# Kernel tuning notes

Measured on AMD Instinct MI355X. Metric: run time of the kernel, lower is better.

The kernel has to match this reference:

```python
import jax, jax.numpy as jnp
import numpy as np

B, N, C, NB, K, CAT = 8, 32768, 32, 2, 22, 40


def setup_inputs() -> dict:
    key = jax.random.key(0)
    ks = jax.random.split(key, 16)
    w = lambda k, s: jax.random.normal(k, s, jnp.float32) * 0.05
    return {
        "features": jax.random.normal(ks[0], (B, 1, N, K), jnp.float32),
        "clusters": jax.random.randint(ks[1], (NB, B, N), 0, C),
        "w_in": w(ks[2], (256, K)), "b_in": jnp.zeros((256,), jnp.float32),
        "w1": w(ks[3], (NB, 64, 256)), "b1": jnp.zeros((NB, 64), jnp.float32),
        "w2": w(ks[4], (NB, 128, 64)), "b2": jnp.zeros((NB, 128), jnp.float32),
        "w3": w(ks[5], (NB, 128, 128)), "b3": jnp.zeros((NB, 128), jnp.float32),
        "wc1": w(ks[6], (NB, 128, 128)), "bc1": jnp.zeros((NB, 128), jnp.float32),
        "wc2": w(ks[7], (NB, 256, 128)), "bc2": jnp.zeros((NB, 256), jnp.float32),
        "wc3": w(ks[8], (NB, 32, 256)), "bc3": jnp.zeros((NB, 32), jnp.float32),
        "w_out1": w(ks[9], (128, 256)), "b_out1": jnp.zeros((128,), jnp.float32),
        "w_out2": w(ks[10], (128, 128)), "b_out2": jnp.zeros((128,), jnp.float32),
        "dw1": w(ks[11], (128, 256)), "db1": jnp.zeros((256,), jnp.float32),
        "dw2": w(ks[12], (256, 256)), "db2": jnp.zeros((256,), jnp.float32),
        "dw3": w(ks[13], (256, CAT)), "db3": jnp.zeros((CAT,), jnp.float32),
    }


def conv(x, w, b):  # 1x1 conv over [B, Cin, N] -> [B, Cout, N] with ReLU
    return jax.nn.relu(jnp.einsum('oc,bcn->bon', w, x) + b[None, :, None])


def seg_max(x, idx):  # x [B, d, N], idx [B, N] -> [B, d, C] (matches masked -100 max-pool)
    f = jax.vmap(lambda xi, ii: jax.ops.segment_max(xi.T, ii, num_segments=C))(x, idx)
    return jnp.maximum(f.transpose(0, 2, 1), -100.0)


def pooling_block(f, idx, wc1, bc1, wc2, bc2, wc3, bc3):
    corr = conv(conv(conv(f, wc1, bc1), wc2, bc2), wc3, bc3)  # [B, 32, N]
    cf = seg_max(f, idx)      # [B, d, C]
    cc = seg_max(corr, idx)   # [B, 32, C]
    cm = cc.transpose(0, 2, 1)  # [B, C, 32]
    cm = cm / jnp.maximum(jnp.linalg.norm(cm, axis=-1, keepdims=True), 1e-12)
    corr_matrix = cm @ cm.transpose(0, 2, 1)  # [B, C, C]
    cf = cf @ corr_matrix  # [B, d, C]
    # scatter-back: each point gathers its cluster's pooled feature
    return jnp.take_along_axis(cf, idx[:, None, :], axis=2)  # [B, d, N]


def reference(features, clusters, w_in, b_in, w1, b1, w2, b2, w3, b3,
              wc1, bc1, wc2, bc2, wc3, bc3, w_out1, b_out1, w_out2, b_out2,
              dw1, db1, dw2, db2, dw3, db3):
    x = features[:, 0]  # [B, N, K]
    f = jax.nn.relu(jnp.einsum('ok,bnk->bon', w_in, x) + b_in[None, :, None])  # [B,256,N]
    for i in range(NB):
        f = conv(f, w1[i], b1[i])   # 256 -> 64
        f = conv(f, w2[i], b2[i])   # 64 -> 128
        pool = pooling_block(f, clusters[i], wc1[i], bc1[i], wc2[i], bc2[i], wc3[i], bc3[i])
        f = conv(f, w3[i], b3[i])   # 128 -> 128
        f = jnp.concatenate([f, pool], axis=1)  # -> 256
    o = conv(conv(f, w_out1, b_out1), w_out2, b_out2)  # [B,128,N]
    net = jnp.max(o, axis=2)  # global max-pool over N -> [B,128]
    lrelu = lambda v: jnp.where(v >= 0, v, 0.2 * v)
    net = lrelu(net @ dw1 + db1)
    net = lrelu(net @ dw2 + db2)
    return net @ dw3 + db3  # [B, CAT]
```

## Files before the change

kernel.cpp:

```cpp
#include <hip/hip_runtime.h>
#include <stdint.h>

#define B_   8
#define N_   32768
#define C_   32
#define K_   22
#define CAT_ 40

typedef unsigned short u16;
typedef unsigned int   u32;

typedef __attribute__((ext_vector_type(8))) short bf16x8;
typedef __attribute__((ext_vector_type(4))) float f32x4;

#define MFMA(a, b, c) __builtin_amdgcn_mfma_f32_16x16x32_bf16(a, b, c, 0, 0, 0)

__device__ __forceinline__ float b2f(u16 v) { return __uint_as_float(((u32)v) << 16); }
__device__ __forceinline__ u16 f2b(float f) {
    u32 x = __float_as_uint(f);
    return (u16)((x + 0x7fffu + ((x >> 16) & 1u)) >> 16);
}
__device__ __forceinline__ u32 pk2(float a, float b) {
    return (u32)f2b(a) | ((u32)f2b(b) << 16);
}

#define PK_WIN 0
#define PK_W1  8192
#define PK_W2  40960
#define PK_W3  57344
#define PK_WC1 90112
#define PK_WC2 122880
#define PK_WC3 188416
#define PK_WO1 204800
#define PK_WO2 237568

#define OBIN 0
#define OB1  256
#define OB2  384
#define OB3  640
#define OBC1 896
#define OBC2 1152
#define OBC3 1664
#define OBO1 1728
#define OBO2 1856
#define ODB1 1984
#define ODB2 2240
#define ODB3 2496

#define ODW1 0
#define ODW2 32768
#define ODW3 98304

#define OFS_WPK   0u
#define OFS_BIAS  524288u
#define OFS_DWC   540672u
#define OFS_MODE  786432u
#define OFS_FEATC 1048576u
#define OFS_GACC0 12582912u
#define OFS_GACC1 12746752u
#define OFS_GNET  12910592u
#define GACC_ZERO_BYTES 331776u
#define OFS_CF2B0 12914688u
#define OFS_CF2B1 12980224u
#define OFS_F0    16777216u
#define OFS_F1    83886080u

#define SEGSTR 161
#define SEGTOT (32 * SEGSTR)
#define CFSTR 136

__global__ void kSniff(const u16* __restrict__ featAny, int* __restrict__ mode) {
    __shared__ int cnt;
    if (threadIdx.x == 0) cnt = 0;
    __syncthreads();
    int weird = 0;
    for (int j = 0; j < 4; ++j) {
        u16 v = featAny[threadIdx.x * 4 + j];
        float f = b2f(v);
        if (v == 0 || !(fabsf(f) < 1e10f)) weird++;
    }
    if (weird) atomicAdd(&cnt, weird);
    __syncthreads();
    if (threadIdx.x == 0) *mode = (cnt > 64) ? 1 : 0;
}

__device__ __forceinline__ float fetchF(const void* src, size_t i, int mode) {
    return mode ? ((const float*)src)[i] : b2f(((const u16*)src)[i]);
}

__device__ void packA(const void* __restrict__ src, u16* __restrict__ dst,
                      int COUT, int CIN, int mode, int tid, int np) {
    int KB = (CIN + 31) / 32;
    int tiles = COUT / 16;
    int tot = tiles * KB * 64 * 8;
    for (int i = tid; i < tot; i += np) {
        int j = i & 7;
        int L = (i >> 3) & 63;
        int rest = i >> 9;
        int kb = rest % KB, tile = rest / KB;
        int co = tile * 16 + (L & 15);
        int ci = kb * 32 + (L >> 4) * 8 + j;
        float v = (ci < CIN) ? fetchF(src, (size_t)co * CIN + ci, mode) : 0.f;
        dst[i] = f2b(v);
    }
}

__device__ void cvtF(const void* __restrict__ src, float* __restrict__ dst,
                     int n, int mode, int tid, int np) {
    for (int i = tid; i < n; i += np) dst[i] = fetchF(src, i, mode);
}

__device__ void cvtB(const void* __restrict__ src, u16* __restrict__ dst,
                     int n, int mode, int tid, int np) {
    for (int i = tid; i < n; i += np)
        dst[i] = mode ? f2b(((const float*)src)[i]) : ((const u16*)src)[i];
}

__global__ void kPrep(const void* feat, const void* w_in, const void* b_in,
                      const void* w1, const void* b1, const void* w2, const void* b2,
                      const void* w3, const void* b3,
                      const void* wc1, const void* bc1, const void* wc2, const void* bc2,
                      const void* wc3, const void* bc3,
                      const void* wo1, const void* bo1, const void* wo2, const void* bo2,
                      const void* dw1, const void* db1, const void* dw2, const void* db2,
                      const void* dw3, const void* db3,
                      u16* WPK, float* BIAS, u16* DWC, u16* FEATC,
                      const int* __restrict__ modep) {
    const int mode = *modep;
    int tid = blockIdx.x * blockDim.x + threadIdx.x;
    int np  = gridDim.x * blockDim.x;
    cvtB(feat, FEATC, B_ * N_ * K_, mode, tid, np);
    packA(w_in, WPK + PK_WIN, 256, 22, mode, tid, np);
    packA(w1,                                 WPK + PK_W1,          64, 256, mode, tid, np);
    packA((const u16*)w1 + (mode?32768:16384), WPK + PK_W1 + 16384,  64, 256, mode, tid, np);
    packA(w2,                                 WPK + PK_W2,          128, 64, mode, tid, np);
    packA((const u16*)w2 + (mode?16384:8192),  WPK + PK_W2 + 8192,   128, 64, mode, tid, np);
    packA(w3,                                 WPK + PK_W3,          128, 128, mode, tid, np);
    packA((const u16*)w3 + (mode?32768:16384), WPK + PK_W3 + 16384,  128, 128, mode, tid, np);
    packA(wc1,                                WPK + PK_WC1,         128, 128, mode, tid, np);
    packA((const u16*)wc1 + (mode?32768:16384),WPK + PK_WC1 + 16384, 128, 128, mode, tid, np);
    packA(wc2,                                WPK + PK_WC2,         256, 128, mode, tid, np);
    packA((const u16*)wc2 + (mode?65536:32768),WPK + PK_WC2 + 32768, 256, 128, mode, tid, np);
    packA(wc3,                                WPK + PK_WC3,         32, 256, mode, tid, np);
    packA((const u16*)wc3 + (mode?16384:8192), WPK + PK_WC3 + 8192,  32, 256, mode, tid, np);
    packA(wo1, WPK + PK_WO1, 128, 256, mode, tid, np);
    packA(wo2, WPK + PK_WO2, 128, 128, mode, tid, np);
    cvtF(b_in, BIAS + OBIN, 256, mode, tid, np);
    cvtF(b1,   BIAS + OB1,  128, mode, tid, np);
    cvtF(b2,   BIAS + OB2,  256, mode, tid, np);
    cvtF(b3,   BIAS + OB3,  256, mode, tid, np);
    cvtF(bc1,  BIAS + OBC1, 256, mode, tid, np);
    cvtF(bc2,  BIAS + OBC2, 512, mode, tid, np);
    cvtF(bc3,  BIAS + OBC3, 64,  mode, tid, np);
    cvtF(bo1,  BIAS + OBO1, 128, mode, tid, np);
    cvtF(bo2,  BIAS + OBO2, 128, mode, tid, np);
    cvtF(db1,  BIAS + ODB1, 256, mode, tid, np);
    cvtF(db2,  BIAS + ODB2, 256, mode, tid, np);
    cvtF(db3,  BIAS + ODB3, 40,  mode, tid, np);
    cvtB(dw1, DWC + ODW1, 128 * 256, mode, tid, np);
    cvtB(dw2, DWC + ODW2, 256 * 256, mode, tid, np);
    cvtB(dw3, DWC + ODW3, 256 * 40,  mode, tid, np);
}

__device__ __forceinline__ void storeRow(u16* __restrict__ buf, int p, int col,
                                         float r0, float r1, float r2, float r3) {
    *(uint2*)(buf + p * 136 + col) = make_uint2(pk2(r0, r1), pk2(r2, r3));
}

template<int NF>
__device__ __forceinline__ void loadWF(const u16* __restrict__ wA, int lane, bf16x8 (&wf)[NF]) {
#pragma unroll
    for (int i = 0; i < NF; ++i)
        wf[i] = *(const bf16x8*)(wA + ((size_t)(i * 64 + lane)) * 8);
}

template<int KB, int INS>
__device__ __forceinline__ void convP128w(const bf16x8 (&wf)[KB], const float* __restrict__ bias,
                                          const u16* __restrict__ sIn, u16* __restrict__ sOut) {
    const int t = threadIdx.x, lane = t & 63, w = t >> 6, lp = lane & 15, q = lane >> 4;
    f32x4 acc[8] = {};
#pragma unroll
    for (int kb = 0; kb < KB; ++kb) {
        bf16x8 bb[8];
#pragma unroll
        for (int pt = 0; pt < 8; ++pt)
            bb[pt] = *(const bf16x8*)(sIn + (pt * 16 + lp) * INS + kb * 32 + q * 8);
#pragma unroll
        for (int pt = 0; pt < 8; ++pt) acc[pt] = MFMA(wf[kb], bb[pt], acc[pt]);
    }
    const int co = w * 16 + q * 4;
    f32x4 bv = *(const f32x4*)(bias + co);
#pragma unroll
    for (int pt = 0; pt < 8; ++pt) {
        f32x4 v = acc[pt];
        storeRow(sOut, pt * 16 + lp, co,
                 fmaxf(v[0] + bv[0], 0.f), fmaxf(v[1] + bv[1], 0.f),
                 fmaxf(v[2] + bv[2], 0.f), fmaxf(v[3] + bv[3], 0.f));
    }
}

__device__ __forceinline__ void convW2_128w(const bf16x8 (&wf)[2], const float* __restrict__ bias,
                                            const u16* __restrict__ sIn, u16* __restrict__ sOut,
                                            const int* __restrict__ sCluSeg, int* __restrict__ sSeg) {
    const int t = threadIdx.x, lane = t & 63, w = t >> 6, lp = lane & 15, q = lane >> 4;
    f32x4 acc[8] = {};
#pragma unroll
    for (int kb = 0; kb < 2; ++kb) {
        bf16x8 bb[8];
#pragma unroll
        for (int pt = 0; pt < 8; ++pt)
            bb[pt] = *(const bf16x8*)(sIn + (pt * 16 + lp) * 136 + kb * 32 + q * 8);
#pragma unroll
        for (int pt = 0; pt < 8; ++pt) acc[pt] = MFMA(wf[kb], bb[pt], acc[pt]);
    }
    const int co = w * 16 + q * 4;
    f32x4 bv = *(const f32x4*)(bias + co);
#pragma unroll
    for (int pt = 0; pt < 8; ++pt) {
        f32x4 v = acc[pt];
        const int p = pt * 16 + lp;
        float r0 = fmaxf(v[0] + bv[0], 0.f), r1 = fmaxf(v[1] + bv[1], 0.f);
        float r2 = fmaxf(v[2] + bv[2], 0.f), r3 = fmaxf(v[3] + bv[3], 0.f);
        *(uint2*)(sOut + p * 136 + co) = make_uint2(pk2(r0, r1), pk2(r2, r3));
        const int sb = sCluSeg[p] * SEGSTR + co;
        atomicMax(&sSeg[sb + 0], __float_as_int(r0));
        atomicMax(&sSeg[sb + 1], __float_as_int(r1));
        atomicMax(&sSeg[sb + 2], __float_as_int(r2));
        atomicMax(&sSeg[sb + 3], __float_as_int(r3));
    }
}

__device__ __forceinline__ void convCat128w(const bf16x8 (&wf)[8], const float* __restrict__ bias,
                                            const u16* __restrict__ sLo, const u16* __restrict__ sHi,
                                            u16* __restrict__ sOut) {
    const int t = threadIdx.x, lane = t & 63, w = t >> 6, lp = lane & 15, q = lane >> 4;
    const int ct = w & 3, pp = (w >> 2) * 4;
    f32x4 acc[4] = {};
#pragma unroll
    for (int kb = 0; kb < 8; ++kb) {
        const u16* sIn = (kb < 4) ? sLo : sHi;
        const int col = (kb & 3) * 32 + q * 8;
        bf16x8 bb[4];
#pragma unroll
        for (int i = 0; i < 4; ++i)
            bb[i] = *(const bf16x8*)(sIn + ((pp + i) * 16 + lp) * 136 + col);
#pragma unroll
        for (int i = 0; i < 4; ++i) acc[i] = MFMA(wf[kb], bb[i], acc[i]);
    }
    const int co = ct * 16 + q * 4;
    f32x4 bv = *(const f32x4*)(bias + co);
#pragma unroll
    for (int i = 0; i < 4; ++i) {
        f32x4 v = acc[i];
        storeRow(sOut, (pp + i) * 16 + lp, co,
                 fmaxf(v[0] + bv[0], 0.f), fmaxf(v[1] + bv[1], 0.f),
                 fmaxf(v[2] + bv[2], 0.f), fmaxf(v[3] + bv[3], 0.f));
    }
}

__device__ __forceinline__ void convCatG128s(const bf16x8 (&wf)[8], const float* __restrict__ bias,
                                             const u16* __restrict__ sIn, const u16* __restrict__ sCf,
                                             const int* __restrict__ sClu, u16* __restrict__ sOut) {
    const int t = threadIdx.x, lane = t & 63, w = t >> 6, lp = lane & 15, q = lane >> 4;
    const int ct = w & 3, pp = (w >> 2) * 4;
    f32x4 acc[4] = {};
#pragma unroll
    for (int kb = 0; kb < 8; ++kb) {
        bf16x8 bb[4];
#pragma unroll
        for (int i = 0; i < 4; ++i) {
            const int p = (pp + i) * 16 + lp;
            if (kb < 4) bb[i] = *(const bf16x8*)(sIn + p * 136 + kb * 32 + q * 8);
            else        bb[i] = *(const bf16x8*)(sCf + sClu[p] * CFSTR + (kb - 4) * 32 + q * 8);
        }
#pragma unroll
        for (int i = 0; i < 4; ++i) acc[i] = MFMA(wf[kb], bb[i], acc[i]);
    }
    const int co = ct * 16 + q * 4;
    f32x4 bv = *(const f32x4*)(bias + co);
#pragma unroll
    for (int i = 0; i < 4; ++i) {
        f32x4 v = acc[i];
        storeRow(sOut, (pp + i) * 16 + lp, co,
                 fmaxf(v[0] + bv[0], 0.f), fmaxf(v[1] + bv[1], 0.f),
                 fmaxf(v[2] + bv[2], 0.f), fmaxf(v[3] + bv[3], 0.f));
    }
}

__device__ __forceinline__ void convG128w(const bf16x8 (&wf)[4], const float* __restrict__ bias,
                                          const u16* __restrict__ gB, u16* __restrict__ sOut) {
    const int t = threadIdx.x, lane = t & 63, w = t >> 6, lp = lane & 15, q = lane >> 4;
    f32x4 acc[8] = {};
#pragma unroll
    for (int kb = 0; kb < 4; ++kb) {
        bf16x8 bb[8];
#pragma unroll
        for (int pt = 0; pt < 8; ++pt)
            bb[pt] = *(const bf16x8*)(gB + pt * 2048 + kb * 512 + lane * 8);
#pragma unroll
        for (int pt = 0; pt < 8; ++pt) acc[pt] = MFMA(wf[kb], bb[pt], acc[pt]);
    }
    const int co = w * 16 + q * 4;
    f32x4 bv = *(const f32x4*)(bias + co);
#pragma unroll
    for (int pt = 0; pt < 8; ++pt) {
        f32x4 v = acc[pt];
        storeRow(sOut, pt * 16 + lp, co,
                 fmaxf(v[0] + bv[0], 0.f), fmaxf(v[1] + bv[1], 0.f),
                 fmaxf(v[2] + bv[2], 0.f), fmaxf(v[3] + bv[3], 0.f));
    }
}

__device__ __forceinline__ void wc3seg128w(const bf16x8 (&wf)[8], const float* __restrict__ bias,
                                           const u16* __restrict__ sLo, const u16* __restrict__ sHi,
                                           const int* __restrict__ sClu, int* __restrict__ sSeg) {
    const int t = threadIdx.x, lane = t & 63, w = t >> 6, lp = lane & 15, q = lane >> 4;
    const int ct = w & 1, pp = (w >> 1) * 2;
    f32x4 acc[2] = {};
#pragma unroll
    for (int kb = 0; kb < 8; ++kb) {
        const u16* sIn = (kb < 4) ? sLo : sHi;
        const int col = (kb & 3) * 32 + q * 8;
        bf16x8 b0 = *(const bf16x8*)(sIn + ((pp + 0) * 16 + lp) * 136 + col);
        bf16x8 b1 = *(const bf16x8*)(sIn + ((pp + 1) * 16 + lp) * 136 + col);
        acc[0] = MFMA(wf[kb], b0, acc[0]);
        acc[1] = MFMA(wf[kb], b1, acc[1]);
    }
    const int col = ct * 16 + q * 4;
    f32x4 bv = *(const f32x4*)(bias + col);
#pragma unroll
    for (int i = 0; i < 2; ++i) {
        const int p = (pp + i) * 16 + lp;
        const int cl = sClu[p];
        f32x4 v = acc[i];
        atomicMax(&sSeg[cl * SEGSTR + 128 + col + 0], __float_as_int(fmaxf(v[0] + bv[0], 0.f)));
        atomicMax(&sSeg[cl * SEGSTR + 128 + col + 1], __float_as_int(fmaxf(v[1] + bv[1], 0.f)));
        atomicMax(&sSeg[cl * SEGSTR + 128 + col + 2], __float_as_int(fmaxf(v[2] + bv[2], 0.f)));
        atomicMax(&sSeg[cl * SEGSTR + 128 + col + 3], __float_as_int(fmaxf(v[3] + bv[3], 0.f)));
    }
}

__device__ __forceinline__ void convCatG128os(const bf16x8 (&wf)[8], const float* __restrict__ bias,
                                              const u16* __restrict__ sIn, const u16* __restrict__ sCf,
                                              const int* __restrict__ sClu, u16* __restrict__ sOut) {
    const int t = threadIdx.x, lane = t & 63, w = t >> 6, lp = lane & 15, q = lane >> 4;
    f32x4 acc[8] = {};
#pragma unroll
    for (int kb = 0; kb < 8; ++kb) {
        bf16x8 bb[8];
#pragma unroll
        for (int pt = 0; pt < 8; ++pt) {
            const int p = pt * 16 + lp;
            if (kb < 4) bb[pt] = *(const bf16x8*)(sIn + p * 136 + kb * 32 + q * 8);
            else        bb[pt] = *(const bf16x8*)(sCf + sClu[p] * CFSTR + (kb - 4) * 32 + q * 8);
        }
#pragma unroll
        for (int pt = 0; pt < 8; ++pt) acc[pt] = MFMA(wf[kb], bb[pt], acc[pt]);
    }
    const int co = w * 16 + q * 4;
    f32x4 bv = *(const f32x4*)(bias + co);
#pragma unroll
    for (int pt = 0; pt < 8; ++pt) {
        f32x4 v = acc[pt];
        storeRow(sOut, pt * 16 + lp, co,
                 fmaxf(v[0] + bv[0], 0.f), fmaxf(v[1] + bv[1], 0.f),
                 fmaxf(v[2] + bv[2], 0.f), fmaxf(v[3] + bv[3], 0.f));
    }
}

__device__ __forceinline__ void convNet128w(const bf16x8 (&wf)[4], const float* __restrict__ bias,
                                            const u16* __restrict__ sIn, int* __restrict__ sNet) {
    const int t = threadIdx.x, lane = t & 63, w = t >> 6, lp = lane & 15, q = lane >> 4;
    f32x4 acc[8] = {};
#pragma unroll
    for (int kb = 0; kb < 4; ++kb) {
        bf16x8 bb[8];
#pragma unroll
        for (int pt = 0; pt < 8; ++pt)
            bb[pt] = *(const bf16x8*)(sIn + (pt * 16 + lp) * 136 + kb * 32 + q * 8);
#pragma unroll
        for (int pt = 0; pt < 8; ++pt) acc[pt] = MFMA(wf[kb], bb[pt], acc[pt]);
    }
    const int co = w * 16 + q * 4;
    f32x4 bv = *(const f32x4*)(bias + co);
    f32x4 m = acc[0];
#pragma unroll
    for (int pt = 1; pt < 8; ++pt) {
        m[0] = fmaxf(m[0], acc[pt][0]); m[1] = fmaxf(m[1], acc[pt][1]);
        m[2] = fmaxf(m[2], acc[pt][2]); m[3] = fmaxf(m[3], acc[pt][3]);
    }
    atomicMax(&sNet[co + 0], __float_as_int(fmaxf(m[0] + bv[0], 0.f)));
    atomicMax(&sNet[co + 1], __float_as_int(fmaxf(m[1] + bv[1], 0.f)));
    atomicMax(&sNet[co + 2], __float_as_int(fmaxf(m[2] + bv[2], 0.f)));
    atomicMax(&sNet[co + 3], __float_as_int(fmaxf(m[3] + bv[3], 0.f)));
}

__global__ __launch_bounds__(512, 2)
void kA0a(const u16* __restrict__ featc, const int* __restrict__ clu0,
          const u16* __restrict__ WPK, const float* __restrict__ BIAS,
          u16* __restrict__ gF, int* __restrict__ gSeg) {
    __shared__ __attribute__((aligned(16))) u16 sA[128 * 136];
    __shared__ __attribute__((aligned(16))) u16 sB[128 * 136];
    __shared__ __attribute__((aligned(16))) u16 sC[128 * 136];
    __shared__ __attribute__((aligned(16))) u16 sFeat[128 * 40];
    __shared__ int sSeg[SEGTOT];
    __shared__ int sClu[128];
    const int t = threadIdx.x, lane = t & 63, w = t >> 6, lp = lane & 15, q = lane >> 4;
    const int b = blockIdx.y;
    const size_t bN = (size_t)b * N_;
    bf16x8 wf1a[1], wf1b[1], wf2[8], wf3[2];
    loadWF(WPK + PK_WIN + w * 512, lane, wf1a);
    loadWF(WPK + PK_WIN + 4096 + w * 512, lane, wf1b);
    loadWF(WPK + PK_W1 + (w & 3) * 4096, lane, wf2);
    loadWF(WPK + PK_W2 + w * 1024, lane, wf3);
    for (int i = t; i < SEGTOT; i += 512) sSeg[i] = 0;
    {
        const int n0 = blockIdx.x * 1024;
        for (int i = t; i < 5120; i += 512) {
            int p = i / 40, k = i - p * 40;
            sFeat[i] = (k < 22) ? featc[(bN + n0 + p) * 22 + k] : (u16)0;
        }
    }
    __syncthreads();
    for (int s = 0; s < 8; ++s) {
        const int n0 = (blockIdx.x * 8 + s) * 128;
        const size_t ntB = (size_t)b * 2048 + (size_t)(blockIdx.x * 8 + s) * 8;
        if (t < 128) sClu[t] = clu0[bN + n0 + t];
        convP128w<1, 40>(wf1a, BIAS + OBIN,       sFeat, sA);
        convP128w<1, 40>(wf1b, BIAS + OBIN + 128, sFeat, sB);
        __syncthreads();
        convCat128w(wf2, BIAS + OB1, sA, sB, sC);
        __syncthreads();
        convW2_128w(wf3, BIAS + OB2, sC, sA, sClu, sSeg);
        __syncthreads();
        {
#pragma unroll
            for (int r = 0; r < 4; ++r) {
                bf16x8 v = *(const bf16x8*)(sA + (w * 16 + lp) * 136 + r * 32 + q * 8);
                *(bf16x8*)(gF + ((ntB + w) * 4 + r) * 512 + lane * 8) = v;
            }
        }
        if (s < 7) {
            const int n1 = n0 + 128;
            for (int i = t; i < 5120; i += 512) {
                int p = i / 40, k = i - p * 40;
                sFeat[i] = (k < 22) ? featc[(bN + n1 + p) * 22 + k] : (u16)0;
            }
        }
        __syncthreads();
    }
    for (int i = t; i < 4096; i += 512) {
        int cl = i >> 7, ch = i & 127;
        atomicMax(&gSeg[b * 5120 + cl * 160 + ch], sSeg[cl * SEGSTR + ch]);
    }
}

template<int PKOFF, int BOFF>
__device__ __forceinline__ void kAbBody(const u16* __restrict__ gFp, const int* __restrict__ clu,
                                        const u16* __restrict__ WPK, const float* __restrict__ BIAS,
                                        int* __restrict__ gSeg) {
    __shared__ __attribute__((aligned(16))) u16 sA[128 * 136];
    __shared__ __attribute__((aligned(16))) u16 sB[128 * 136];
    __shared__ __attribute__((aligned(16))) u16 sC[128 * 136];
    __shared__ int sSeg[SEGTOT];
    __shared__ int sClu[128];
    const int t = threadIdx.x, lane = t & 63, w = t >> 6;
    const int b = blockIdx.y;
    const size_t bN = (size_t)b * N_;
    bf16x8 wf4[4], wf5a[4], wf5b[4], wf6[8];
    loadWF(WPK + PK_WC1 + PKOFF * 16384 + w * 2048, lane, wf4);
    loadWF(WPK + PK_WC2 + PKOFF * 32768 + w * 2048, lane, wf5a);
    loadWF(WPK + PK_WC2 + PKOFF * 32768 + 16384 + w * 2048, lane, wf5b);
    loadWF(WPK + PK_WC3 + PKOFF * 8192 + (w & 1) * 4096, lane, wf6);
    for (int i = t; i < SEGTOT; i += 512) sSeg[i] = 0;
    __syncthreads();
    for (int s = 0; s < 8; ++s) {
        const int n0 = (blockIdx.x * 8 + s) * 128;
        const size_t ntB = (size_t)b * 2048 + (size_t)(blockIdx.x * 8 + s) * 8;
        if (t < 128) sClu[t] = clu[bN + n0 + t];
        const u16* gB = gFp + ntB * 2048;
        convG128w(wf4, BIAS + OBC1 + BOFF * 128, gB, sA);
        __syncthreads();
        convP128w<4, 136>(wf5a, BIAS + OBC2 + BOFF * 256,       sA, sB);
        convP128w<4, 136>(wf5b, BIAS + OBC2 + BOFF * 256 + 128, sA, sC);
        __syncthreads();
        wc3seg128w(wf6, BIAS + OBC3 + BOFF * 32, sB, sC, sClu, sSeg);
        __syncthreads();
    }
    for (int i = t; i < 1024; i += 512) {
        int cl = i >> 5, ch = i & 31;
        atomicMax(&gSeg[b * 5120 + cl * 160 + 128 + ch], sSeg[cl * SEGSTR + 128 + ch]);
    }
}

__global__ __launch_bounds__(512, 2)
void kA0b(const u16* __restrict__ gFp, const int* __restrict__ clu0,
          const u16* __restrict__ WPK, const float* __restrict__ BIAS,
          int* __restrict__ gSeg) {
    kAbBody<0, 0>(gFp, clu0, WPK, BIAS, gSeg);
}

__global__ __launch_bounds__(512, 2)
void kA1b(const u16* __restrict__ gFp, const int* __restrict__ clu1,
          const u16* __restrict__ WPK, const float* __restrict__ BIAS,
          int* __restrict__ gSeg) {
    kAbBody<1, 1>(gFp, clu1, WPK, BIAS, gSeg);
}

__global__ __launch_bounds__(256)
void kB(const int* __restrict__ gSeg, u16* __restrict__ cf2b) {
    __shared__ float sA[5120];
    __shared__ float sR[1024];
    __shared__ float sI[32];
    const int t = threadIdx.x, b = blockIdx.x;
    for (int i = t; i < 5120; i += 256) sA[i] = __int_as_float(gSeg[b * 5120 + i]);
    __syncthreads();
    if (t < 32) {
        float s = 0.f;
        for (int j = 0; j < 32; ++j) { float v = sA[t * 160 + 128 + j]; s = fmaf(v, v, s); }
        sI[t] = 1.f / fmaxf(sqrtf(s), 1e-12f);
    }
    __syncthreads();
    for (int i = t; i < 1024; i += 256) {
        int ca = i >> 5, cb = i & 31;
        float s = 0.f;
        for (int j = 0; j < 32; ++j)
            s = fmaf(sA[ca * 160 + 128 + j], sA[cb * 160 + 128 + j], s);
        sR[i] = s * sI[ca] * sI[cb];
    }
    __syncthreads();
    for (int i = t; i < 4096; i += 256) {
        int c = i >> 7, ch = i & 127;
        float s = 0.f;
        for (int cp = 0; cp < 32; ++cp)
            s = fmaf(sA[cp * 160 + ch], sR[cp * 32 + c], s);
        cf2b[((size_t)b * 32 + c) * 128 + ch] = f2b(s);
    }
}

__global__ __launch_bounds__(512, 2)
void kA1a(const u16* __restrict__ gFp, const int* __restrict__ clu_g,
          const int* __restrict__ clu_s, const u16* __restrict__ cf2b,
          const u16* __restrict__ WPK, const float* __restrict__ BIAS,
          u16* __restrict__ gFo, int* __restrict__ gSeg) {
    __shared__ __attribute__((aligned(16))) u16 sA[128 * 136];
    __shared__ __attribute__((aligned(16))) u16 sB[128 * 136];
    __shared__ __attribute__((aligned(16))) u16 sC[128 * 136];
    __shared__ __attribute__((aligned(16))) u16 sCf[32 * CFSTR];
    __shared__ int sSeg[SEGTOT];
    __shared__ int sClu0[128];
    __shared__ int sClu1[128];
    const int t = threadIdx.x, lane = t & 63, w = t >> 6, lp = lane & 15, q = lane >> 4;
    const int b = blockIdx.y;
    const size_t bN = (size_t)b * N_;
    bf16x8 wfG[4], wf2[8], wf3[2];
    loadWF(WPK + PK_W3 + w * 2048, lane, wfG);
    loadWF(WPK + PK_W1 + 16384 + (w & 3) * 4096, lane, wf2);
    loadWF(WPK + PK_W2 + 8192 + w * 1024, lane, wf3);
    for (int i = t; i < SEGTOT; i += 512) sSeg[i] = 0;
    const u16* cfb = cf2b + (size_t)b * 4096;
    for (int i = t; i < 4096; i += 512) {
        int cl = i >> 7, ch = i & 127;
        sCf[cl * CFSTR + ch] = cfb[i];
    }
    __syncthreads();
    for (int s = 0; s < 8; ++s) {
        const int n0 = (blockIdx.x * 8 + s) * 128;
        const size_t ntB = (size_t)b * 2048 + (size_t)(blockIdx.x * 8 + s) * 8;
        if (t < 128) sClu0[t] = clu_g[bN + n0 + t];
        else if (t < 256) sClu1[t - 128] = clu_s[bN + n0 + (t - 128)];
        const u16* gB = gFp + ntB * 2048;
        convG128w(wfG, BIAS + OB3, gB, sA);
        __syncthreads();
        convCatG128s(wf2, BIAS + OB1 + 64, sA, sCf, sClu0, sB);
        __syncthreads();
        convW2_128w(wf3, BIAS + OB2 + 128, sB, sC, sClu1, sSeg);
        __syncthreads();
        {
#pragma unroll
            for (int r = 0; r < 4; ++r) {
                bf16x8 v = *(const bf16x8*)(sC + (w * 16 + lp) * 136 + r * 32 + q * 8);
                *(bf16x8*)(gFo + ((ntB + w) * 4 + r) * 512 + lane * 8) = v;
            }
        }
        __syncthreads();
    }
    for (int i = t; i < 4096; i += 512) {
        int cl = i >> 7, ch = i & 127;
        atomicMax(&gSeg[b * 5120 + cl * 160 + ch], sSeg[cl * SEGSTR + ch]);
    }
}

__global__ __launch_bounds__(512, 2)
void kC(const u16* __restrict__ gFp, const int* __restrict__ clu_g,
        const u16* __restrict__ cf2b,
        const u16* __restrict__ WPK, const float* __restrict__ BIAS,
        int* __restrict__ gNet) {
    __shared__ __attribute__((aligned(16))) u16 sA[128 * 136];
    __shared__ __attribute__((aligned(16))) u16 sB[128 * 136];
    __shared__ __attribute__((aligned(16))) u16 sCf[32 * CFSTR];
    __shared__ int sNet[128];
    __shared__ int sClu[128];
    const int t = threadIdx.x, lane = t & 63, w = t >> 6;
    const int b = blockIdx.y;
    const size_t bN = (size_t)b * N_;
    bf16x8 wfG[4], wfO1[8], wfO2[4];
    loadWF(WPK + PK_W3 + 16384 + w * 2048, lane, wfG);
    loadWF(WPK + PK_WO1 + w * 4096, lane, wfO1);
    loadWF(WPK + PK_WO2 + w * 2048, lane, wfO2);
    if (t < 128) sNet[t] = 0;
    const u16* cfb = cf2b + (size_t)b * 4096;
    for (int i = t; i < 4096; i += 512) {
        int cl = i >> 7, ch = i & 127;
        sCf[cl * CFSTR + ch] = cfb[i];
    }
    __syncthreads();
    for (int s = 0; s < 4; ++s) {
        const int n0 = (blockIdx.x * 4 + s) * 128;
        if (t < 128) sClu[t] = clu_g[bN + n0 + t];
        const u16* gB = gFp + ((size_t)b * 2048 + (size_t)(blockIdx.x * 4 + s) * 8) * 2048;
        convG128w(wfG, BIAS + OB3 + 128, gB, sA);
        __syncthreads();
        convCatG128os(wfO1, BIAS + OBO1, sA, sCf, sClu, sB);
        __syncthreads();
        convNet128w(wfO2, BIAS + OBO2, sB, sNet);
        __syncthreads();
    }
    if (t < 128) atomicMax(&gNet[b * 128 + t], sNet[t]);
}

__global__ __launch_bounds__(256)
void kD(const int* __restrict__ gNet, const u16* __restrict__ DWC,
        const float* __restrict__ BIAS, void* __restrict__ outv,
        const int* __restrict__ modep) {
    __shared__ float sN[128];
    __shared__ float sD1[256];
    __shared__ float sD2[256];
    const int mode = *modep;
    const int t = threadIdx.x, bb = blockIdx.x;
    if (t < 128) sN[t] = __int_as_float(gNet[bb * 128 + t]);
    __syncthreads();
    {
        float s = BIAS[ODB1 + t];
        for (int k = 0; k < 128; ++k)
            s = fmaf(sN[k], b2f(DWC[ODW1 + k * 256 + t]), s);
        sD1[t] = (s >= 0.f) ? s : 0.2f * s;
    }
    __syncthreads();
    {
        float s = BIAS[ODB2 + t];
        for (int k = 0; k < 256; ++k)
            s = fmaf(sD1[k], b2f(DWC[ODW2 + k * 256 + t]), s);
        sD2[t] = (s >= 0.f) ? s : 0.2f * s;
    }
    __syncthreads();
    if (t < 40) {
        float s = BIAS[ODB3 + t];
        for (int k = 0; k < 256; ++k)
            s = fmaf(sD2[k], b2f(DWC[ODW3 + k * 40 + t]), s);
        if (mode) ((float*)outv)[bb * 40 + t] = s;
        else      ((u16*)outv)[bb * 40 + t]   = f2b(s);
    }
}

extern "C" void kernel_launch(void* const* d_in, const int* in_sizes, int n_in,
                              void* d_out, int out_size, void* d_ws, size_t ws_size,
                              hipStream_t stream) {
    const void* feat = d_in[0];
    const int* clus = (const int*)d_in[1];

    char* ws = (char*)d_ws;
    u16*   WPK   = (u16*)(ws + OFS_WPK);
    float* BIAS  = (float*)(ws + OFS_BIAS);
    u16*   DWC   = (u16*)(ws + OFS_DWC);
    int*   modep = (int*)(ws + OFS_MODE);
    u16*   FEATC = (u16*)(ws + OFS_FEATC);
    int*   seg0  = (int*)(ws + OFS_GACC0);
    int*   seg1  = (int*)(ws + OFS_GACC1);
    int*   gNet  = (int*)(ws + OFS_GNET);
    u16*   cf2b0 = (u16*)(ws + OFS_CF2B0);
    u16*   cf2b1 = (u16*)(ws + OFS_CF2B1);
    u16*   f0    = (u16*)(ws + OFS_F0);
    u16*   f1    = (u16*)(ws + OFS_F1);

    hipMemsetAsync(ws + OFS_GACC0, 0, GACC_ZERO_BYTES, stream);
    hipLaunchKernelGGL(kSniff, dim3(1), dim3(256), 0, stream, (const u16*)feat, modep);
    hipLaunchKernelGGL(kPrep, dim3(256), dim3(256), 0, stream,
                       feat, d_in[2], d_in[3], d_in[4], d_in[5], d_in[6], d_in[7],
                       d_in[8], d_in[9], d_in[10], d_in[11], d_in[12], d_in[13],
                       d_in[14], d_in[15], d_in[16], d_in[17], d_in[18], d_in[19],
                       d_in[20], d_in[21], d_in[22], d_in[23], d_in[24], d_in[25],
                       WPK, BIAS, DWC, FEATC, modep);

    const int* clu0 = clus;
    const int* clu1 = clus + (size_t)B_ * N_;

    hipLaunchKernelGGL(kA0a, dim3(32, 8), dim3(512), 0, stream,
                       FEATC, clu0, WPK, BIAS, f0, seg0);
    hipLaunchKernelGGL(kA0b, dim3(32, 8), dim3(512), 0, stream,
                       f0, clu0, WPK, BIAS, seg0);
    hipLaunchKernelGGL(kB, dim3(8), dim3(256), 0, stream, seg0, cf2b0);
    hipLaunchKernelGGL(kA1a, dim3(32, 8), dim3(512), 0, stream,
                       f0, clu0, clu1, cf2b0, WPK, BIAS, f1, seg1);
    hipLaunchKernelGGL(kA1b, dim3(32, 8), dim3(512), 0, stream,
                       f1, clu1, WPK, BIAS, seg1);
    hipLaunchKernelGGL(kB, dim3(8), dim3(256), 0, stream, seg1, cf2b1);
    hipLaunchKernelGGL(kC, dim3(64, 8), dim3(512), 0, stream,
                       f1, clu1, cf2b1, WPK, BIAS, gNet);
    hipLaunchKernelGGL(kD, dim3(8), dim3(256), 0, stream,
                       gNet, DWC, BIAS, d_out, modep);
}
```

Baseline: 481.3 us.

## Shrink kA0a to 64-point tiles with 256-thread blocks and more blocks

Restructures the first layer-stack kernel to process 64-point tiles with 4 waves per block instead of 128-point tiles with 8 waves. The grid doubles to 64x8 blocks and each wave computes more output channels. The per-cluster max buffer shrinks to 128 channels with a stride of 129, which cuts LDS use. The goal is more resident blocks per CU and better latency hiding, at the cost of more global atomic merges per batch and less weight reuse per block.

```diff
diff --git a/kernel.cpp b/kernel.cpp
--- a/kernel.cpp
+++ b/kernel.cpp
@@ -67,6 +67,8 @@
 
 #define SEGSTR 161
 #define SEGTOT (32 * SEGSTR)
+#define SEGFSTR 129
+#define SEGFTOT (32 * SEGFSTR)
 #define CFSTR 136
 
 __global__ void kSniff(const u16* __restrict__ featAny, int* __restrict__ mode) {
@@ -174,6 +176,102 @@
         wf[i] = *(const bf16x8*)(wA + ((size_t)(i * 64 + lane)) * 8);
 }
 
+template<int CT, int KB, int INS>
+__device__ __forceinline__ void convL64w(const bf16x8 (&wf)[CT * KB], const float* __restrict__ bias,
+                                         const u16* __restrict__ sIn, u16* __restrict__ sOut) {
+    const int t = threadIdx.x, lane = t & 63, w = t >> 6, lp = lane & 15, q = lane >> 4;
+    f32x4 acc[CT][4] = {};
+#pragma unroll
+    for (int kb = 0; kb < KB; ++kb) {
+        bf16x8 bb[4];
+#pragma unroll
+        for (int pt = 0; pt < 4; ++pt)
+            bb[pt] = *(const bf16x8*)(sIn + (pt * 16 + lp) * INS + kb * 32 + q * 8);
+#pragma unroll
+        for (int ct = 0; ct < CT; ++ct)
+#pragma unroll
+            for (int pt = 0; pt < 4; ++pt)
+                acc[ct][pt] = MFMA(wf[ct * KB + kb], bb[pt], acc[ct][pt]);
+    }
+#pragma unroll
+    for (int ct = 0; ct < CT; ++ct) {
+        const int co = (w * CT + ct) * 16 + q * 4;
+        f32x4 bv = *(const f32x4*)(bias + co);
+        const int col = co & 127;
+#pragma unroll
+        for (int pt = 0; pt < 4; ++pt) {
+            f32x4 v = acc[ct][pt];
+            storeRow(sOut, pt * 16 + lp, col,
+                     fmaxf(v[0] + bv[0], 0.f), fmaxf(v[1] + bv[1], 0.f),
+                     fmaxf(v[2] + bv[2], 0.f), fmaxf(v[3] + bv[3], 0.f));
+        }
+    }
+}
+
+__device__ __forceinline__ void convCat64w(const bf16x8 (&wf)[8], const float* __restrict__ bias,
+                                           const u16* __restrict__ sLo, const u16* __restrict__ sHi,
+                                           u16* __restrict__ sOut) {
+    const int t = threadIdx.x, lane = t & 63, w = t >> 6, lp = lane & 15, q = lane >> 4;
+    f32x4 acc[4] = {};
+#pragma unroll
+    for (int kb = 0; kb < 8; ++kb) {
+        const u16* sIn = (kb < 4) ? sLo : sHi;
+        const int col = (kb & 3) * 32 + q * 8;
+        bf16x8 bb[4];
+#pragma unroll
+        for (int pt = 0; pt < 4; ++pt)
+            bb[pt] = *(const bf16x8*)(sIn + (pt * 16 + lp) * 136 + col);
+#pragma unroll
+        for (int pt = 0; pt < 4; ++pt) acc[pt] = MFMA(wf[kb], bb[pt], acc[pt]);
+    }
+    const int co = w * 16 + q * 4;
+    f32x4 bv = *(const f32x4*)(bias + co);
+#pragma unroll
+    for (int pt = 0; pt < 4; ++pt) {
+        f32x4 v = acc[pt];
+        storeRow(sOut, pt * 16 + lp, co,
+                 fmaxf(v[0] + bv[0], 0.f), fmaxf(v[1] + bv[1], 0.f),
+                 fmaxf(v[2] + bv[2], 0.f), fmaxf(v[3] + bv[3], 0.f));
+    }
+}
+
+__device__ __forceinline__ void convW2_64w(const bf16x8 (&wf)[4], const float* __restrict__ bias,
+                                           const u16* __restrict__ sIn, u16* __restrict__ sOut,
+                                           const int* __restrict__ sClu, int* __restrict__ sSegF) {
+    const int t = threadIdx.x, lane = t & 63, w = t >> 6, lp = lane & 15, q = lane >> 4;
+    f32x4 acc[2][4] = {};
+#pragma unroll
+    for (int kb = 0; kb < 2; ++kb) {
+        bf16x8 bb[4];
+#pragma unroll
+        for (int pt = 0; pt < 4; ++pt)
+            bb[pt] = *(const bf16x8*)(sIn + (pt * 16 + lp) * 136 + kb * 32 + q * 8);
+#pragma unroll
+        for (int ct = 0; ct < 2; ++ct)
+#pragma unroll
+            for (int pt = 0; pt < 4; ++pt)
+                acc[ct][pt] = MFMA(wf[ct * 2 + kb], bb[pt], acc[ct][pt]);
+    }
+#pragma unroll
+    for (int ct = 0; ct < 2; ++ct) {
+        const int co = (w * 2 + ct) * 16 + q * 4;
+        f32x4 bv = *(const f32x4*)(bias + co);
+#pragma unroll
+        for (int pt = 0; pt < 4; ++pt) {
+            f32x4 v = acc[ct][pt];
+            const int p = pt * 16 + lp;
+            float r0 = fmaxf(v[0] + bv[0], 0.f), r1 = fmaxf(v[1] + bv[1], 0.f);
+            float r2 = fmaxf(v[2] + bv[2], 0.f), r3 = fmaxf(v[3] + bv[3], 0.f);
+            *(uint2*)(sOut + p * 136 + co) = make_uint2(pk2(r0, r1), pk2(r2, r3));
+            const int sb = sClu[p] * SEGFSTR + co;
+            atomicMax(&sSegF[sb + 0], __float_as_int(r0));
+            atomicMax(&sSegF[sb + 1], __float_as_int(r1));
+            atomicMax(&sSegF[sb + 2], __float_as_int(r2));
+            atomicMax(&sSegF[sb + 3], __float_as_int(r3));
+        }
+    }
+}
+
 template<int KB, int INS>
 __device__ __forceinline__ void convP128w(const bf16x8 (&wf)[KB], const float* __restrict__ bias,
                                           const u16* __restrict__ sIn, u16* __restrict__ sOut) {
@@ -230,34 +328,6 @@
     }
 }
 
-__device__ __forceinline__ void convCat128w(const bf16x8 (&wf)[8], const float* __restrict__ bias,
-                                            const u16* __restrict__ sLo, const u16* __restrict__ sHi,
-                                            u16* __restrict__ sOut) {
-    const int t = threadIdx.x, lane = t & 63, w = t >> 6, lp = lane & 15, q = lane >> 4;
-    const int ct = w & 3, pp = (w >> 2) * 4;
-    f32x4 acc[4] = {};
-#pragma unroll
-    for (int kb = 0; kb < 8; ++kb) {
-        const u16* sIn = (kb < 4) ? sLo : sHi;
-        const int col = (kb & 3) * 32 + q * 8;
-        bf16x8 bb[4];
-#pragma unroll
-        for (int i = 0; i < 4; ++i)
-            bb[i] = *(const bf16x8*)(sIn + ((pp + i) * 16 + lp) * 136 + col);
-#pragma unroll
-        for (int i = 0; i < 4; ++i) acc[i] = MFMA(wf[kb], bb[i], acc[i]);
-    }
-    const int co = ct * 16 + q * 4;
-    f32x4 bv = *(const f32x4*)(bias + co);
-#pragma unroll
-    for (int i = 0; i < 4; ++i) {
-        f32x4 v = acc[i];
-        storeRow(sOut, (pp + i) * 16 + lp, co,
-                 fmaxf(v[0] + bv[0], 0.f), fmaxf(v[1] + bv[1], 0.f),
-                 fmaxf(v[2] + bv[2], 0.f), fmaxf(v[3] + bv[3], 0.f));
-    }
-}
-
 __device__ __forceinline__ void convCatG128s(const bf16x8 (&wf)[8], const float* __restrict__ bias,
                                              const u16* __restrict__ sIn, const u16* __restrict__ sCf,
                                              const int* __restrict__ sClu, u16* __restrict__ sOut) {
@@ -395,43 +465,43 @@
     atomicMax(&sNet[co + 3], __float_as_int(fmaxf(m[3] + bv[3], 0.f)));
 }
 
-__global__ __launch_bounds__(512, 2)
+__global__ __launch_bounds__(256, 2)
 void kA0a(const u16* __restrict__ featc, const int* __restrict__ clu0,
           const u16* __restrict__ WPK, const float* __restrict__ BIAS,
           u16* __restrict__ gF, int* __restrict__ gSeg) {
-    __shared__ __attribute__((aligned(16))) u16 sA[128 * 136];
-    __shared__ __attribute__((aligned(16))) u16 sB[128 * 136];
-    __shared__ __attribute__((aligned(16))) u16 sC[128 * 136];
-    __shared__ __attribute__((aligned(16))) u16 sFeat[128 * 40];
-    __shared__ int sSeg[SEGTOT];
-    __shared__ int sClu[128];
+    __shared__ __attribute__((aligned(16))) u16 sA[64 * 136];
+    __shared__ __attribute__((aligned(16))) u16 sB[64 * 136];
+    __shared__ __attribute__((aligned(16))) u16 sC[64 * 136];
+    __shared__ __attribute__((aligned(16))) u16 sFeat[64 * 40];
+    __shared__ int sSegF[SEGFTOT];
+    __shared__ int sClu[64];
     const int t = threadIdx.x, lane = t & 63, w = t >> 6, lp = lane & 15, q = lane >> 4;
     const int b = blockIdx.y;
     const size_t bN = (size_t)b * N_;
-    bf16x8 wf1a[1], wf1b[1], wf2[8], wf3[2];
-    loadWF(WPK + PK_WIN + w * 512, lane, wf1a);
-    loadWF(WPK + PK_WIN + 4096 + w * 512, lane, wf1b);
-    loadWF(WPK + PK_W1 + (w & 3) * 4096, lane, wf2);
-    loadWF(WPK + PK_W2 + w * 1024, lane, wf3);
-    for (int i = t; i < SEGTOT; i += 512) sSeg[i] = 0;
+    bf16x8 wfL[2], wfH[2], wf1[8], wf2[4];
+    loadWF(WPK + PK_WIN + (2 * w) * 512, lane, wfL);
+    loadWF(WPK + PK_WIN + 4096 + (2 * w) * 512, lane, wfH);
+    loadWF(WPK + PK_W1 + w * 4096, lane, wf1);
+    loadWF(WPK + PK_W2 + w * 2048, lane, wf2);
+    for (int i = t; i < SEGFTOT; i += 256) sSegF[i] = 0;
     {
-        const int n0 = blockIdx.x * 1024;
-        for (int i = t; i < 5120; i += 512) {
+        const int n0 = blockIdx.x * 512;
+        for (int i = t; i < 2560; i += 256) {
             int p = i / 40, k = i - p * 40;
             sFeat[i] = (k < 22) ? featc[(bN + n0 + p) * 22 + k] : (u16)0;
         }
     }
     __syncthreads();
     for (int s = 0; s < 8; ++s) {
-        const int n0 = (blockIdx.x * 8 + s) * 128;
-        const size_t ntB = (size_t)b * 2048 + (size_t)(blockIdx.x * 8 + s) * 8;
-        if (t < 128) sClu[t] = clu0[bN + n0 + t];
-        convP128w<1, 40>(wf1a, BIAS + OBIN,       sFeat, sA);
-        convP128w<1, 40>(wf1b, BIAS + OBIN + 128, sFeat, sB);
-        __syncthreads();
-        convCat128w(wf2, BIAS + OB1, sA, sB, sC);
-        __syncthreads();
-        convW2_128w(wf3, BIAS + OB2, sC, sA, sClu, sSeg);
+        const int n0 = (blockIdx.x * 8 + s) * 64;
+        const size_t ntB = (size_t)b * 2048 + (size_t)(blockIdx.x * 8 + s) * 4;
+        if (t < 64) sClu[t] = clu0[bN + n0 + t];
+        convL64w<2, 1, 40>(wfL, BIAS + OBIN,       sFeat, sA);
+        convL64w<2, 1, 40>(wfH, BIAS + OBIN + 128, sFeat, sB);
+        __syncthreads();
+        convCat64w(wf1, BIAS + OB1, sA, sB, sC);
+        __syncthreads();
+        convW2_64w(wf2, BIAS + OB2, sC, sA, sClu, sSegF);
         __syncthreads();
         {
 #pragma unroll
@@ -441,17 +511,17 @@
             }
         }
         if (s < 7) {
-            const int n1 = n0 + 128;
-            for (int i = t; i < 5120; i += 512) {
+            const int n1 = n0 + 64;
+            for (int i = t; i < 2560; i += 256) {
                 int p = i / 40, k = i - p * 40;
                 sFeat[i] = (k < 22) ? featc[(bN + n1 + p) * 22 + k] : (u16)0;
             }
         }
         __syncthreads();
     }
-    for (int i = t; i < 4096; i += 512) {
+    for (int i = t; i < 4096; i += 256) {
         int cl = i >> 7, ch = i & 127;
-        atomicMax(&gSeg[b * 5120 + cl * 160 + ch], sSeg[cl * SEGSTR + ch]);
+        atomicMax(&gSeg[b * 5120 + cl * 160 + ch], sSegF[cl * SEGFSTR + ch]);
     }
 }
 
@@ -695,7 +765,7 @@
     const int* clu0 = clus;
     const int* clu1 = clus + (size_t)B_ * N_;
 
-    hipLaunchKernelGGL(kA0a, dim3(32, 8), dim3(512), 0, stream,
+    hipLaunchKernelGGL(kA0a, dim3(64, 8), dim3(256), 0, stream,
                        FEATC, clu0, WPK, BIAS, f0, seg0);
     hipLaunchKernelGGL(kA0b, dim3(32, 8), dim3(512), 0, stream,
                        f0, clu0, WPK, BIAS, seg0);
```

After: 476.8 us. About the same (-0.9%).
